# Performance work log

Hardware: AMD Instinct MI355X
Metric: run time of the kernel (lower is better)

The kernel has to match this reference:

```python
import jax, jax.numpy as jnp
import numpy as np
from jax import lax


def affine_grid(theta, H, W):
    # theta [2,3]; torch F.affine_grid, align_corners=False (pixel centers)
    xs = (jnp.arange(W, dtype=jnp.float32) * 2 + 1) / W - 1
    ys = (jnp.arange(H, dtype=jnp.float32) * 2 + 1) / H - 1
    gx, gy = jnp.meshgrid(xs, ys)  # [H,W]
    base = jnp.stack([gx, gy, jnp.ones_like(gx)], -1)  # [H,W,3]
    return jnp.einsum('hwk,jk->hwj', base, theta)  # [H,W,2]


def grid_sample(img, grid):
    # img [C,H,W], grid [H,W,2] normalized; bilinear, zero padding, align_corners=False
    C, H, W = img.shape
    x = ((grid[..., 0] + 1) * W - 1) * 0.5
    y = ((grid[..., 1] + 1) * H - 1) * 0.5
    x0 = jnp.floor(x); y0 = jnp.floor(y)
    x1 = x0 + 1; y1 = y0 + 1
    wx1 = x - x0; wx0 = 1 - wx1
    wy1 = y - y0; wy0 = 1 - wy1
    def gather(xi, yi):
        xic = jnp.clip(xi, 0, W - 1).astype(jnp.int32)
        yic = jnp.clip(yi, 0, H - 1).astype(jnp.int32)
        valid = ((xi >= 0) & (xi <= W - 1) & (yi >= 0) & (yi <= H - 1)).astype(img.dtype)
        return img[:, yic, xic] * valid  # [C,H,W]
    return (gather(x0, y0) * (wx0 * wy0) + gather(x1, y0) * (wx1 * wy0)
            + gather(x0, y1) * (wx0 * wy1) + gather(x1, y1) * (wx1 * wy1))


def warp_one(feat, t):
    # feat [C,H,W], t [4,4]: rotate then translate, two bilinear resamples (as in source)
    C, H, W = feat.shape
    zero = jnp.zeros((), feat.dtype); one = jnp.ones((), feat.dtype)
    theta_rot = jnp.stack([jnp.stack([t[0, 0], t[0, 1], zero]),
                           jnp.stack([t[1, 0], t[1, 1], zero])])
    x_tr = 4 * t[0, 3] / 128
    y_tr = -(4 * t[1, 3]) / 128
    theta_tr = jnp.stack([jnp.stack([one, zero, x_tr]),
                          jnp.stack([zero, one, y_tr])])
    f = grid_sample(feat, affine_grid(theta_rot, H, W))
    return grid_sample(f, affine_grid(theta_tr, H, W))


def conv2d(x, w, b):
    y = lax.conv_general_dilated(x, w, (1, 1), 'SAME',
                                 dimension_numbers=('NCHW', 'OIHW', 'NCHW'))
    return y + b[None, :, None, None]


def convgru_step0(x, wx, wh, bx, bh):
    # single-layer ConvGRU, one timestep, h0 = 0 => hidden convs vanish, only bh remains
    C = wh.shape[1]
    gx = conv2d(x, wx, bx)  # [N,3C,H,W]
    xr, xz, xn = jnp.split(gx, 3, axis=1)
    br, bz, bn = jnp.split(bh, 3)
    r = jax.nn.sigmoid(xr + br[None, :, None, None])
    z = jax.nn.sigmoid(xz + bz[None, :, None, None])
    n = jnp.tanh(xn + r * bn[None, :, None, None])
    return (1 - z) * n  # h' = (1-z)*n + z*0


def setup_inputs() -> dict:
    key = jax.random.key(0)
    ks = jax.random.split(key, 6)
    B, A, C, H, W = 2, 5, 64, 128, 128
    feats = jax.random.normal(ks[0], (B, A, C, H, W), jnp.float32)
    ang = jax.random.uniform(ks[1], (B, A, A), minval=-np.pi, maxval=np.pi).astype(jnp.float32)
    ca, sa = jnp.cos(ang), jnp.sin(ang)
    t = jnp.zeros((B, A, A, 4, 4), jnp.float32)
    t = t.at[..., 0, 0].set(ca).at[..., 0, 1].set(-sa)
    t = t.at[..., 1, 0].set(sa).at[..., 1, 1].set(ca)
    tr = jax.random.uniform(ks[2], (B, A, A, 2), minval=-10.0, maxval=10.0)
    t = t.at[..., 0, 3].set(tr[..., 0]).at[..., 1, 3].set(tr[..., 1])
    wx = jax.random.normal(ks[3], (3 * C, 2 * C, 3, 3), jnp.float32) * 0.05
    wh = jax.random.normal(ks[4], (3 * C, C, 3, 3), jnp.float32) * 0.05
    bx = jnp.zeros((3 * C,), jnp.float32)
    bh = jnp.zeros((3 * C,), jnp.float32)
    return {'feats': feats, 'trans': t, 'wx': wx, 'wh': wh, 'bx': bx, 'bh': bh,
            'num_agent': A, 'gnn_iter': 2}


def reference(feats, trans, wx, wh, bx, bh, num_agent, gnn_iter):
    trans = lax.stop_gradient(trans)  # source builds theta via torch.tensor (detached)
    B, A, C, H, W = feats.shape
    mask = 1.0 - jnp.eye(A, dtype=feats.dtype)  # exclude self (j != i)
    warp = jax.vmap(jax.vmap(jax.vmap(warp_one, (0, 0)), (None, 0)), (0, 0))
    for _ in range(gnn_iter):
        warped = warp(feats, trans)  # [B, A_i, A_j, C, H, W]
        mean = jnp.einsum('bijchw,ij->bichw', warped, mask) / (A - 1)
        cat = jnp.concatenate([feats, mean], axis=2).reshape(B * A, 2 * C, H, W)
        feats = convgru_step0(cat, wx, wh, bx, bh).reshape(B, A, C, H, W)
    return feats
```

## Files before the change

kernel.cpp:

```cpp
#include <hip/hip_runtime.h>
#include <cmath>

#define BB 2
#define AA 5
#define CH 64
#define HH 128
#define WW 128
#define HW (HH*WW)
#define NIMG (BB*AA)

typedef __attribute__((ext_vector_type(8))) _Float16 half8;
typedef __attribute__((ext_vector_type(2))) _Float16 half2v;
typedef __attribute__((ext_vector_type(4))) float floatx4;
typedef unsigned int uint32;
typedef __attribute__((ext_vector_type(4))) uint32 uint4v;

__device__ inline half8 hzero() {
    half8 v;
#pragma unroll
    for (int e = 0; e < 8; ++e) v[e] = (_Float16)0.f;
    return v;
}

__device__ inline float fsigmoid(float x) {
    return __builtin_amdgcn_rcpf(1.f + __builtin_amdgcn_exp2f(-1.442695041f * x));
}
__device__ inline float ftanh(float x) {
    return 2.f * fsigmoid(2.f * x) - 1.f;
}

__global__ __launch_bounds__(256) void to_nhwc_kernel(
    const float* __restrict__ src, _Float16* __restrict__ dst)
{
    const int img = blockIdx.y;
    const int cg  = blockIdx.x & 7;
    const int pb  = blockIdx.x >> 3;
    const int p   = pb * 256 + threadIdx.x;
    const float* s = src + ((size_t)img * CH + cg * 8) * HW + p;
    half8 v;
#pragma unroll
    for (int e = 0; e < 8; ++e) v[e] = (_Float16)s[e * HW];
    *(half8*)(dst + ((size_t)img * HW + p) * 128 + cg * 8) = v;
}

__global__ __launch_bounds__(256) void pack_w_kernel(
    const float* __restrict__ wx, half8* __restrict__ wp)
{
    int idx = blockIdx.x * 256 + threadIdx.x;
    if (idx >= 4 * 9 * 4 * 192) return;
    int oc = idx % 192; int r = idx / 192;
    int gk = r & 3; r >>= 2; int tap = r % 9; int cc = r / 9;
    int ky = tap / 3, kx = tap % 3;
    half8 v;
#pragma unroll
    for (int e = 0; e < 8; ++e)
        v[e] = (_Float16)wx[(((size_t)oc * 128 + cc * 32 + gk * 8 + e) * 3 + ky) * 3 + kx];
    wp[idx] = v;
}

__global__ __launch_bounds__(256, 5) void warp_mean_kernel(
    const _Float16* __restrict__ nh,
    const float* __restrict__ trans,
    _Float16* __restrict__ nhw)
{
    __shared__ uint32 f_lds[32 * 9 * 18];

    const int tile = blockIdx.x;
    const int tx0 = (tile & 7) * 16;
    const int ty0 = (tile >> 3) * 8;
    const int bi  = blockIdx.z;
    const int b   = bi / AA, i = bi % AA;
    const int tid = threadIdx.x;

    const int slc = tid & 7;
    const int ptb = tid >> 3;
    const int col = tid & 15;
    const int row = (tid >> 4) & 7;
    const int chh = tid >> 7;

    half2v acc[16];
#pragma unroll
    for (int c = 0; c < 16; ++c) acc[c] = (half2v)(_Float16)0.f;

    for (int j = 0; j < AA; ++j) {
        if (j == i) continue;
        const float* t = trans + (((size_t)b * AA + i) * AA + j) * 16;
        const float t00 = t[0], t01 = t[1], t03 = t[3];
        const float t10 = t[4], t11 = t[5], t13 = t[7];
        const float dxs = 2.f * t03;
        const float dys = -2.f * t13;
        const float sxf = floorf(dxs), syf = floorf(dys);
        const int sx = (int)sxf, sy = (int)syf;
        const float fx = dxs - sxf, fy = dys - syf;
        const _Float16* srcj = nh + (size_t)(b * AA + j) * HW * 128 + slc * 8;

        __syncthreads();
#pragma unroll
        for (int it = 0; it < 5; ++it) {
            const int pt = it * 32 + ptb;
            if (pt < 153) {
                const int prow = pt / 17;
                const int pcol = pt - prow * 17;
                const int qx = tx0 + sx + pcol;
                const int qy = ty0 + sy + prow;
                float e[8];
#pragma unroll
                for (int k = 0; k < 8; ++k) e[k] = 0.f;
                if (((unsigned)qx < (unsigned)WW) & ((unsigned)qy < (unsigned)HH)) {
                    const float xn = (2 * qx + 1) * (1.0f / WW) - 1.f;
                    const float yn = (2 * qy + 1) * (1.0f / HH) - 1.f;
                    const float px = 64.f * (t00 * xn + t01 * yn) + 63.5f;
                    const float py = 64.f * (t10 * xn + t11 * yn) + 63.5f;
                    const float x0f = floorf(px), y0f = floorf(py);
                    const int x0 = (int)x0f, y0 = (int)y0f;
                    const float wx1 = px - x0f, wx0 = 1.f - wx1;
                    const float wy1 = py - y0f, wy0 = 1.f - wy1;
                    const bool vx0 = (x0 >= 0) & (x0 < WW);
                    const bool vx1 = (x0 + 1 >= 0) & (x0 + 1 < WW);
                    const bool vy0 = (y0 >= 0) & (y0 < HH);
                    const bool vy1 = (y0 + 1 >= 0) & (y0 + 1 < HH);
                    const int cx0 = min(max(x0, 0), WW - 1);
                    const int cx1 = min(max(x0 + 1, 0), WW - 1);
                    const int cy0 = min(max(y0, 0), HH - 1);
                    const int cy1 = min(max(y0 + 1, 0), HH - 1);
                    const float w00 = (vx0 & vy0) ? wx0 * wy0 : 0.f;
                    const float w01 = (vx1 & vy0) ? wx1 * wy0 : 0.f;
                    const float w10 = (vx0 & vy1) ? wx0 * wy1 : 0.f;
                    const float w11 = (vx1 & vy1) ? wx1 * wy1 : 0.f;
                    const half8 A = *(const half8*)(srcj + ((size_t)cy0 * WW + cx0) * 128);
                    const half8 Bv = *(const half8*)(srcj + ((size_t)cy0 * WW + cx1) * 128);
                    const half8 Cv = *(const half8*)(srcj + ((size_t)cy1 * WW + cx0) * 128);
                    const half8 D = *(const half8*)(srcj + ((size_t)cy1 * WW + cx1) * 128);
#pragma unroll
                    for (int k = 0; k < 8; ++k)
                        e[k] = w00 * (float)A[k] + w01 * (float)Bv[k]
                             + w10 * (float)Cv[k] + w11 * (float)D[k];
                }
                const int lb = slc * 4 * 162 + prow * 18 + pcol;
#pragma unroll
                for (int k = 0; k < 4; ++k) {
                    half2v p;
                    p[0] = (_Float16)e[2 * k];
                    p[1] = (_Float16)e[2 * k + 1];
                    f_lds[lb + k * 162] = __builtin_bit_cast(uint32, p);
                }
            }
        }
        __syncthreads();

        const float wAf = (1.f - fx) * (1.f - fy);
        const float wBf = fx * (1.f - fy);
        const float wCf = (1.f - fx) * fy;
        const float wDf = fx * fy;
        half2v wA2 = (half2v)(_Float16)wAf;
        half2v wB2 = (half2v)(_Float16)wBf;
        half2v wC2 = (half2v)(_Float16)wCf;
        half2v wD2 = (half2v)(_Float16)wDf;
        const uint32* fp0 = f_lds + (chh * 16) * 162 + row * 18 + col;
#pragma unroll
        for (int c = 0; c < 16; ++c) {
            const uint32* fp = fp0 + c * 162;
            const half2v v00 = __builtin_bit_cast(half2v, fp[0]);
            const half2v v01 = __builtin_bit_cast(half2v, fp[1]);
            const half2v v10 = __builtin_bit_cast(half2v, fp[18]);
            const half2v v11 = __builtin_bit_cast(half2v, fp[19]);
            acc[c] += v00 * wA2 + v01 * wB2 + v10 * wC2 + v11 * wD2;
        }
    }

    const half2v q = (half2v)(_Float16)0.25f;
    uint32 os[16];
#pragma unroll
    for (int c = 0; c < 16; ++c) os[c] = __builtin_bit_cast(uint32, acc[c] * q);
    uint4v* dst = (uint4v*)(nhw + ((size_t)bi * HW + (ty0 + row) * WW + tx0 + col) * 128
                            + 64 + chh * 32);
#pragma unroll
    for (int k = 0; k < 4; ++k)
        dst[k] = (uint4v){os[4 * k], os[4 * k + 1], os[4 * k + 2], os[4 * k + 3]};
}

#define APL2 180

__global__ __launch_bounds__(512, 4) void conv_gru_mfma(
    const _Float16* __restrict__ in,
    const half8* __restrict__ wp,
    const float* __restrict__ bx,
    const float* __restrict__ bh,
    float* __restrict__ out_f32,
    _Float16* __restrict__ out_f16)
{
    __shared__ half8 lds_in[16 * APL2];

    const int tid = threadIdx.x;
    const int img = blockIdx.z;
    const int x0 = (blockIdx.x & 7) * 16;
    const int y0 = (blockIdx.x >> 3) * 8;
    const int w   = tid >> 6;
    const int wo  = w & 3;
    const int wh  = w >> 2;
    const int ln  = tid & 15;
    const int kq  = (tid & 63) >> 4;

    const _Float16* inimg = in + (size_t)img * HW * 128;
    for (int f = tid; f < 2880; f += 512) {
        const int g = f / 180; const int r = f % 180;
        const int row = r / 18; const int col = r % 18;
        const int y = y0 + row - 1, x = x0 + col - 1;
        half8 v = hzero();
        if ((unsigned)x < (unsigned)WW && (unsigned)y < (unsigned)HH)
            v = *(const half8*)(inimg + ((size_t)y * WW + x) * 128 + g * 8);
        lds_in[f] = v;
    }

    floatx4 acc[4][3];
#pragma unroll
    for (int s = 0; s < 4; ++s)
#pragma unroll
        for (int t = 0; t < 3; ++t)
#pragma unroll
            for (int r = 0; r < 4; ++r) acc[s][t][r] = 0.f;

    __syncthreads();

    const half8* wbase = wp + kq * 192 + wo * 16 + ln;
    half8 bp0[3], bp1[3];
#pragma unroll
    for (int t = 0; t < 3; ++t) bp0[t] = wbase[t * 64];
#pragma unroll
    for (int t = 0; t < 3; ++t) bp1[t] = wbase[768 + t * 64];

#pragma unroll
    for (int s = 0; s < 36; ++s) {
        const int cc = s / 9, tap = s - cc * 9;
        const int dy = tap / 3, dx = tap - dy * 3;
        half8 bcur[3];
#pragma unroll
        for (int t = 0; t < 3; ++t) { bcur[t] = bp0[t]; bp0[t] = bp1[t]; }
        if (s + 2 < 36) {
            const half8* wsrc = wbase + (size_t)(s + 2) * 768;
#pragma unroll
            for (int t = 0; t < 3; ++t) bp1[t] = wsrc[t * 64];
        }
        half8 a[4];
#pragma unroll
        for (int t = 0; t < 4; ++t)
            a[t] = lds_in[(cc * 4 + kq) * APL2 + (wh * 4 + t + dy) * 18 + ln + dx];
#pragma unroll
        for (int t = 0; t < 4; ++t)
#pragma unroll
            for (int u = 0; u < 3; ++u)
                acc[t][u] = __builtin_amdgcn_mfma_f32_16x16x32_f16(a[t], bcur[u], acc[t][u], 0, 0, 0);
    }

    const int c = wo * 16 + ln;
    const float bxr = bx[c] + bh[c];
    const float bxz = bx[64 + c] + bh[64 + c];
    const float bxn = bx[128 + c];
    const float bnn = bh[128 + c];
#pragma unroll
    for (int s = 0; s < 4; ++s) {
        const int y = y0 + wh * 4 + s;
#pragma unroll
        for (int reg = 0; reg < 4; ++reg) {
            const int x = x0 + kq * 4 + reg;
            const float xr = acc[s][0][reg] + bxr;
            const float xz = acc[s][1][reg] + bxz;
            const float xn = acc[s][2][reg] + bxn;
            const float rg = fsigmoid(xr);
            const float zg = fsigmoid(xz);
            const float n  = ftanh(xn + rg * bnn);
            const float h  = (1.f - zg) * n;
            if (out_f32)
                out_f32[((size_t)img * CH + c) * HW + y * WW + x] = h;
            else
                out_f16[((size_t)img * HW + y * WW + x) * 128 + c] = (_Float16)h;
        }
    }
}

extern "C" void kernel_launch(void* const* d_in, const int* in_sizes, int n_in,
                              void* d_out, int out_size, void* d_ws, size_t ws_size,
                              hipStream_t stream) {
    const float* feats = (const float*)d_in[0];
    const float* trans = (const float*)d_in[1];
    const float* wx    = (const float*)d_in[2];
    const float* bx    = (const float*)d_in[4];
    const float* bh    = (const float*)d_in[5];
    float* out = (float*)d_out;

    char* ws = (char*)d_ws;
    half8*    wpack = (half8*)ws;
    _Float16* B1 = (_Float16*)(ws + 442368);
    _Float16* B2 = (_Float16*)(ws + 442368 + (size_t)NIMG * HW * 128 * 2);

    pack_w_kernel<<<108, 256, 0, stream>>>(wx, wpack);
    to_nhwc_kernel<<<dim3(512, NIMG), 256, 0, stream>>>(feats, B1);

    dim3 wgrid(128, 1, NIMG);
    dim3 cgrid(128, 1, NIMG);

    warp_mean_kernel<<<wgrid, 256, 0, stream>>>(B1, trans, B1);
    conv_gru_mfma<<<cgrid, 512, 0, stream>>>(B1, wpack, bx, bh, nullptr, B2);
    warp_mean_kernel<<<wgrid, 256, 0, stream>>>(B2, trans, B2);
    conv_gru_mfma<<<cgrid, 512, 0, stream>>>(B2, wpack, bx, bh, out, nullptr);
}
```

Before: 328.7 us.

## Fuse warp-mean into ConvGRU conv kernel, computing halo mean in LDS

Merges the warp/mean kernel into the MFMA conv kernel. Each block now computes the warped neighbour mean for its 18x10 halo tile directly into shared memory, so the mean channels never go to global memory. Activations shrink to 64 channels per pixel. This removes a kernel launch and the global write and read of the mean half of the 128-channel buffer. In exchange the warp work for the halo is recomputed, the block carries more LDS, and the bilinear step now runs over 512 threads in half8 vectors.

```diff
diff --git a/kernel.cpp b/kernel.cpp
--- a/kernel.cpp
+++ b/kernel.cpp
@@ -10,10 +10,8 @@
 #define NIMG (BB*AA)
 
 typedef __attribute__((ext_vector_type(8))) _Float16 half8;
-typedef __attribute__((ext_vector_type(2))) _Float16 half2v;
 typedef __attribute__((ext_vector_type(4))) float floatx4;
 typedef unsigned int uint32;
-typedef __attribute__((ext_vector_type(4))) uint32 uint4v;
 
 __device__ inline half8 hzero() {
     half8 v;
@@ -40,7 +38,7 @@
     half8 v;
 #pragma unroll
     for (int e = 0; e < 8; ++e) v[e] = (_Float16)s[e * HW];
-    *(half8*)(dst + ((size_t)img * HW + p) * 128 + cg * 8) = v;
+    *(half8*)(dst + ((size_t)img * HW + p) * 64 + cg * 8) = v;
 }
 
 __global__ __launch_bounds__(256) void pack_w_kernel(
@@ -58,29 +56,48 @@
     wp[idx] = v;
 }
 
-__global__ __launch_bounds__(256, 5) void warp_mean_kernel(
-    const _Float16* __restrict__ nh,
+#define APL2 180
+
+__global__ __launch_bounds__(512, 4) void fused_warp_conv(
+    const _Float16* __restrict__ in,
     const float* __restrict__ trans,
-    _Float16* __restrict__ nhw)
+    const half8* __restrict__ wp,
+    const float* __restrict__ bx,
+    const float* __restrict__ bh,
+    float* __restrict__ out_f32,
+    _Float16* __restrict__ out_f16)
 {
-    __shared__ uint32 f_lds[32 * 9 * 18];
-
-    const int tile = blockIdx.x;
-    const int tx0 = (tile & 7) * 16;
-    const int ty0 = (tile >> 3) * 8;
+    __shared__ half8 lds_in[16 * APL2];
+    __shared__ half8 f_lds[209 * 8];
+
+    const int tid = threadIdx.x;
     const int bi  = blockIdx.z;
     const int b   = bi / AA, i = bi % AA;
-    const int tid = threadIdx.x;
-
+    const int x0 = (blockIdx.x & 7) * 16;
+    const int y0 = (blockIdx.x >> 3) * 8;
+
+    const int w   = tid >> 6;
+    const int wo  = w & 3;
+    const int wh  = w >> 2;
+    const int ln  = tid & 15;
+    const int kq  = (tid & 63) >> 4;
     const int slc = tid & 7;
     const int ptb = tid >> 3;
-    const int col = tid & 15;
-    const int row = (tid >> 4) & 7;
-    const int chh = tid >> 7;
-
-    half2v acc[16];
-#pragma unroll
-    for (int c = 0; c < 16; ++c) acc[c] = (half2v)(_Float16)0.f;
+
+    const _Float16* inimg = in + (size_t)bi * HW * 64;
+    for (int f = tid; f < 1440; f += 512) {
+        const int g = f / 180; const int r = f % 180;
+        const int row = r / 18; const int col = r % 18;
+        const int y = y0 + row - 1, x = x0 + col - 1;
+        half8 v = hzero();
+        if ((unsigned)x < (unsigned)WW && (unsigned)y < (unsigned)HH)
+            v = *(const half8*)(inimg + ((size_t)y * WW + x) * 64 + g * 8);
+        lds_in[g * APL2 + r] = v;
+    }
+
+    half8 macc[3];
+#pragma unroll
+    for (int k2 = 0; k2 < 3; ++k2) macc[k2] = hzero();
 
     for (int j = 0; j < AA; ++j) {
         if (j == i) continue;
@@ -92,17 +109,17 @@
         const float sxf = floorf(dxs), syf = floorf(dys);
         const int sx = (int)sxf, sy = (int)syf;
         const float fx = dxs - sxf, fy = dys - syf;
-        const _Float16* srcj = nh + (size_t)(b * AA + j) * HW * 128 + slc * 8;
+        const _Float16* srcj = in + (size_t)(b * AA + j) * HW * 64 + slc * 8;
 
         __syncthreads();
 #pragma unroll
-        for (int it = 0; it < 5; ++it) {
-            const int pt = it * 32 + ptb;
-            if (pt < 153) {
-                const int prow = pt / 17;
-                const int pcol = pt - prow * 17;
-                const int qx = tx0 + sx + pcol;
-                const int qy = ty0 + sy + prow;
+        for (int it = 0; it < 4; ++it) {
+            const int pt = it * 64 + ptb;
+            if (pt < 209) {
+                const int prow = pt / 19;
+                const int pcol = pt - prow * 19;
+                const int qx = x0 - 1 + sx + pcol;
+                const int qy = y0 - 1 + sy + prow;
                 float e[8];
 #pragma unroll
                 for (int k = 0; k < 8; ++k) e[k] = 0.f;
@@ -112,104 +129,69 @@
                     const float px = 64.f * (t00 * xn + t01 * yn) + 63.5f;
                     const float py = 64.f * (t10 * xn + t11 * yn) + 63.5f;
                     const float x0f = floorf(px), y0f = floorf(py);
-                    const int x0 = (int)x0f, y0 = (int)y0f;
+                    const int ix0 = (int)x0f, iy0 = (int)y0f;
                     const float wx1 = px - x0f, wx0 = 1.f - wx1;
                     const float wy1 = py - y0f, wy0 = 1.f - wy1;
-                    const bool vx0 = (x0 >= 0) & (x0 < WW);
-                    const bool vx1 = (x0 + 1 >= 0) & (x0 + 1 < WW);
-                    const bool vy0 = (y0 >= 0) & (y0 < HH);
-                    const bool vy1 = (y0 + 1 >= 0) & (y0 + 1 < HH);
-                    const int cx0 = min(max(x0, 0), WW - 1);
-                    const int cx1 = min(max(x0 + 1, 0), WW - 1);
-                    const int cy0 = min(max(y0, 0), HH - 1);
-                    const int cy1 = min(max(y0 + 1, 0), HH - 1);
+                    const bool vx0 = (ix0 >= 0) & (ix0 < WW);
+                    const bool vx1 = (ix0 + 1 >= 0) & (ix0 + 1 < WW);
+                    const bool vy0 = (iy0 >= 0) & (iy0 < HH);
+                    const bool vy1 = (iy0 + 1 >= 0) & (iy0 + 1 < HH);
+                    const int cx0 = min(max(ix0, 0), WW - 1);
+                    const int cx1 = min(max(ix0 + 1, 0), WW - 1);
+                    const int cy0 = min(max(iy0, 0), HH - 1);
+                    const int cy1 = min(max(iy0 + 1, 0), HH - 1);
                     const float w00 = (vx0 & vy0) ? wx0 * wy0 : 0.f;
                     const float w01 = (vx1 & vy0) ? wx1 * wy0 : 0.f;
                     const float w10 = (vx0 & vy1) ? wx0 * wy1 : 0.f;
                     const float w11 = (vx1 & vy1) ? wx1 * wy1 : 0.f;
-                    const half8 A = *(const half8*)(srcj + ((size_t)cy0 * WW + cx0) * 128);
-                    const half8 Bv = *(const half8*)(srcj + ((size_t)cy0 * WW + cx1) * 128);
-                    const half8 Cv = *(const half8*)(srcj + ((size_t)cy1 * WW + cx0) * 128);
-                    const half8 D = *(const half8*)(srcj + ((size_t)cy1 * WW + cx1) * 128);
+                    const half8 A  = *(const half8*)(srcj + ((size_t)cy0 * WW + cx0) * 64);
+                    const half8 Bv = *(const half8*)(srcj + ((size_t)cy0 * WW + cx1) * 64);
+                    const half8 Cv = *(const half8*)(srcj + ((size_t)cy1 * WW + cx0) * 64);
+                    const half8 D  = *(const half8*)(srcj + ((size_t)cy1 * WW + cx1) * 64);
 #pragma unroll
                     for (int k = 0; k < 8; ++k)
                         e[k] = w00 * (float)A[k] + w01 * (float)Bv[k]
                              + w10 * (float)Cv[k] + w11 * (float)D[k];
                 }
-                const int lb = slc * 4 * 162 + prow * 18 + pcol;
-#pragma unroll
-                for (int k = 0; k < 4; ++k) {
-                    half2v p;
-                    p[0] = (_Float16)e[2 * k];
-                    p[1] = (_Float16)e[2 * k + 1];
-                    f_lds[lb + k * 162] = __builtin_bit_cast(uint32, p);
-                }
+                half8 p;
+#pragma unroll
+                for (int k = 0; k < 8; ++k) p[k] = (_Float16)e[k];
+                f_lds[pt * 8 + slc] = p;
             }
         }
         __syncthreads();
 
-        const float wAf = (1.f - fx) * (1.f - fy);
-        const float wBf = fx * (1.f - fy);
-        const float wCf = (1.f - fx) * fy;
-        const float wDf = fx * fy;
-        half2v wA2 = (half2v)(_Float16)wAf;
-        half2v wB2 = (half2v)(_Float16)wBf;
-        half2v wC2 = (half2v)(_Float16)wCf;
-        half2v wD2 = (half2v)(_Float16)wDf;
-        const uint32* fp0 = f_lds + (chh * 16) * 162 + row * 18 + col;
-#pragma unroll
-        for (int c = 0; c < 16; ++c) {
-            const uint32* fp = fp0 + c * 162;
-            const half2v v00 = __builtin_bit_cast(half2v, fp[0]);
-            const half2v v01 = __builtin_bit_cast(half2v, fp[1]);
-            const half2v v10 = __builtin_bit_cast(half2v, fp[18]);
-            const half2v v11 = __builtin_bit_cast(half2v, fp[19]);
-            acc[c] += v00 * wA2 + v01 * wB2 + v10 * wC2 + v11 * wD2;
-        }
-    }
-
-    const half2v q = (half2v)(_Float16)0.25f;
-    uint32 os[16];
-#pragma unroll
-    for (int c = 0; c < 16; ++c) os[c] = __builtin_bit_cast(uint32, acc[c] * q);
-    uint4v* dst = (uint4v*)(nhw + ((size_t)bi * HW + (ty0 + row) * WW + tx0 + col) * 128
-                            + 64 + chh * 32);
-#pragma unroll
-    for (int k = 0; k < 4; ++k)
-        dst[k] = (uint4v){os[4 * k], os[4 * k + 1], os[4 * k + 2], os[4 * k + 3]};
-}
-
-#define APL2 180
-
-__global__ __launch_bounds__(512, 4) void conv_gru_mfma(
-    const _Float16* __restrict__ in,
-    const half8* __restrict__ wp,
-    const float* __restrict__ bx,
-    const float* __restrict__ bh,
-    float* __restrict__ out_f32,
-    _Float16* __restrict__ out_f16)
-{
-    __shared__ half8 lds_in[16 * APL2];
-
-    const int tid = threadIdx.x;
-    const int img = blockIdx.z;
-    const int x0 = (blockIdx.x & 7) * 16;
-    const int y0 = (blockIdx.x >> 3) * 8;
-    const int w   = tid >> 6;
-    const int wo  = w & 3;
-    const int wh  = w >> 2;
-    const int ln  = tid & 15;
-    const int kq  = (tid & 63) >> 4;
-
-    const _Float16* inimg = in + (size_t)img * HW * 128;
-    for (int f = tid; f < 2880; f += 512) {
-        const int g = f / 180; const int r = f % 180;
-        const int row = r / 18; const int col = r % 18;
-        const int y = y0 + row - 1, x = x0 + col - 1;
-        half8 v = hzero();
-        if ((unsigned)x < (unsigned)WW && (unsigned)y < (unsigned)HH)
-            v = *(const half8*)(inimg + ((size_t)y * WW + x) * 128 + g * 8);
-        lds_in[f] = v;
+        const half8 wA8 = (half8)(_Float16)((1.f - fx) * (1.f - fy));
+        const half8 wB8 = (half8)(_Float16)(fx * (1.f - fy));
+        const half8 wC8 = (half8)(_Float16)((1.f - fx) * fy);
+        const half8 wD8 = (half8)(_Float16)(fx * fy);
+#pragma unroll
+        for (int k2 = 0; k2 < 3; ++k2) {
+            const int item = tid + 512 * k2;
+            if (item < 1440) {
+                const int px = item >> 3, g = item & 7;
+                const int row = px / 18, col = px - row * 18;
+                const half8* fp = &f_lds[(row * 19 + col) * 8 + g];
+                macc[k2] += fp[0] * wA8 + fp[8] * wB8 + fp[152] * wC8 + fp[160] * wD8;
+            }
+        }
+    }
+
+    {
+        const half8 q8 = (half8)(_Float16)0.25f;
+#pragma unroll
+        for (int k2 = 0; k2 < 3; ++k2) {
+            const int item = tid + 512 * k2;
+            if (item < 1440) {
+                const int px = item >> 3, g = item & 7;
+                const int row = px / 18, col = px - row * 18;
+                const int y = y0 + row - 1, x = x0 + col - 1;
+                half8 v = hzero();
+                if ((unsigned)x < (unsigned)WW && (unsigned)y < (unsigned)HH)
+                    v = macc[k2] * q8;
+                lds_in[(8 + g) * APL2 + row * 18 + col] = v;
+            }
+        }
     }
 
     floatx4 acc[4][3];
@@ -271,9 +253,9 @@
             const float n  = ftanh(xn + rg * bnn);
             const float h  = (1.f - zg) * n;
             if (out_f32)
-                out_f32[((size_t)img * CH + c) * HW + y * WW + x] = h;
+                out_f32[((size_t)bi * CH + c) * HW + y * WW + x] = h;
             else
-                out_f16[((size_t)img * HW + y * WW + x) * 128 + c] = (_Float16)h;
+                out_f16[((size_t)bi * HW + y * WW + x) * 64 + c] = (_Float16)h;
         }
     }
 }
@@ -291,16 +273,13 @@
     char* ws = (char*)d_ws;
     half8*    wpack = (half8*)ws;
     _Float16* B1 = (_Float16*)(ws + 442368);
-    _Float16* B2 = (_Float16*)(ws + 442368 + (size_t)NIMG * HW * 128 * 2);
+    _Float16* B2 = (_Float16*)(ws + 442368 + (size_t)NIMG * HW * 64 * 2);
 
     pack_w_kernel<<<108, 256, 0, stream>>>(wx, wpack);
     to_nhwc_kernel<<<dim3(512, NIMG), 256, 0, stream>>>(feats, B1);
 
-    dim3 wgrid(128, 1, NIMG);
-    dim3 cgrid(128, 1, NIMG);
-
-    warp_mean_kernel<<<wgrid, 256, 0, stream>>>(B1, trans, B1);
-    conv_gru_mfma<<<cgrid, 512, 0, stream>>>(B1, wpack, bx, bh, nullptr, B2);
-    warp_mean_kernel<<<wgrid, 256, 0, stream>>>(B2, trans, B2);
-    conv_gru_mfma<<<cgrid, 512, 0, stream>>>(B2, wpack, bx, bh, out, nullptr);
-}
+    dim3 fgrid(128, 1, NIMG);
+
+    fused_warp_conv<<<fgrid, 512, 0, stream>>>(B1, trans, wpack, bx, bh, nullptr, B2);
+    fused_warp_conv<<<fgrid, 512, 0, stream>>>(B2, trans, wpack, bx, bh, out, nullptr);
+}
```

Result: faster. 312.5 us (-5.0%).
